# Optimization experiments

Measured on AMD Instinct MI355X. Metric: run time of the kernel, lower is better.

Reference implementation:

```python
import jax, jax.numpy as jnp
import numpy as np
import math

B, C, H, W, M = 8, 256, 128, 128, 7
EPS = 1e-08


def setup_inputs() -> dict:
    key = jax.random.key(0)
    ks = jax.random.split(key, 7)
    x_high = jax.random.normal(ks[0], (B, C, H // 2, W // 2), jnp.float32)
    x_low = jax.random.normal(ks[1], (B, C, H, W), jnp.float32)
    w1 = jax.random.normal(ks[2], (32, M * M), jnp.float32) / np.sqrt(M * M)
    b1 = jnp.zeros((32,), jnp.float32)
    w2 = jax.random.normal(ks[3], (3, 32), jnp.float32) / np.sqrt(32)
    b2 = jnp.zeros((3,), jnp.float32)
    refine_w = jax.random.normal(ks[4], (C, C), jnp.float32) / np.sqrt(C)
    return {"x_high": x_high, "x_low": x_low, "w1": w1, "b1": b1,
            "w2": w2, "b2": b2, "refine_w": refine_w}


def _anisotropic_kernel(params):
    # params: (B,3) -> normalized Gaussian kernels (B, m, m)
    theta = jnp.arctan2(params[:, 0], params[:, 1]) / 2.0 + math.pi / 2.0
    lam1 = jnp.exp(params[:, 2])
    lam2 = 1.0 / (lam1 + EPS)
    coords = jnp.arange(M, dtype=jnp.float32) - (M // 2)  # -3..3
    yy = coords[:, None]  # (m,1) varies along rows (torch meshgrid 'ij')
    xx = coords[None, :]  # (1,m)
    cos_t = jnp.cos(theta)[:, None, None]
    sin_t = jnp.sin(theta)[:, None, None]
    x_rot = xx * cos_t + yy * sin_t          # (B,m,m)
    y_rot = -xx * sin_t + yy * cos_t
    l1 = lam1[:, None, None]
    l2 = lam2[:, None, None]
    k = jnp.exp(-(x_rot ** 2 / (2.0 * l1 ** 2) + y_rot ** 2 / (2.0 * l2 ** 2)))
    return k / (jnp.sum(k, axis=(1, 2), keepdims=True) + EPS)


def _depthwise(x, kern):
    # x: (B,C,H,W), kern: (B,m,m) -> per-sample depthwise conv, kernel shared across C
    k = jnp.repeat(kern, C, axis=0)[:, None, :, :]  # (B*C,1,m,m)
    pad = M // 2
    y = jax.lax.conv_general_dilated(
        x.reshape(1, B * C, H, W), k, (1, 1), [(pad, pad), (pad, pad)],
        dimension_numbers=("NCHW", "OIHW", "NCHW"), feature_group_count=B * C)
    return y.reshape(B, C, H, W)


def reference(x_high, x_low, w1, b1, w2, b2, refine_w):
    # bilinear upsample (align_corners=False == half-pixel, matches jax.image.resize)
    x_high_up = jax.image.resize(x_high, (B, C, H, W), method="bilinear")

    x_f = jnp.fft.fftshift(jnp.fft.fft2(x_low, norm="ortho"), axes=(-2, -1))
    real, imag = jnp.real(x_f), jnp.imag(x_f)
    mag = jnp.abs(x_f)
    mag_weighted = jnp.mean(mag, axis=1, keepdims=True)  # (B,1,H,W)
    h0, w0 = H // 2 - M // 2, W // 2 - M // 2
    mag_center = mag_weighted[:, :, h0:h0 + M, w0:w0 + M]  # (B,1,m,m)

    # param_net: Flatten -> Linear -> ReLU -> Linear
    flat = mag_center.reshape(B, M * M)
    h = jax.nn.relu(flat @ w1.T + b1)
    params = h @ w2.T + b2  # (B,3)

    kern = _anisotropic_kernel(params)
    real_f = _depthwise(real, kern)
    imag_f = _depthwise(imag, kern)

    # 1x1 refine conv (bias-free), shared for real and imag parts
    real_f = jnp.einsum("bchw,oc->bohw", real_f, refine_w)
    imag_f = jnp.einsum("bchw,oc->bohw", imag_f, refine_w)

    out_f = jax.lax.complex(real_f, imag_f)
    out_f = jnp.fft.ifftshift(out_f, axes=(-2, -1))
    x_low_enhanced = jnp.real(jnp.fft.ifft2(out_f, norm="ortho"))
    return x_low_enhanced + x_high_up
```

## Files before the change

### kernel.cpp

```cpp
#include <hip/hip_runtime.h>

typedef __attribute__((ext_vector_type(8))) short bf16x8;
typedef __attribute__((ext_vector_type(4))) float f32x4;
typedef __attribute__((ext_vector_type(4))) int   i32x4;

#define PI_F 3.14159265358979323846f
#define C128 0.0490873852123405f
#define INV_SQRT128 0.0883883476483184f
#define INV128 0.0078125f

#define NB 8
#define NC 256
#define NH 128
#define NW 128
#define IMG 16384
#define NIMG 2048

#define GH_STRIDE 3200
#define AB_STRIDE 3072

__device__ __forceinline__ unsigned short f2bf(float f){
  unsigned int u = __float_as_uint(f);
  u += 0x7FFFu + ((u >> 16) & 1u);
  return (unsigned short)(u >> 16);
}
__device__ __forceinline__ float bf2f(unsigned short u){
  return __uint_as_float(((unsigned int)u) << 16);
}

__device__ __constant__ int c_pcnt[6] = {1,2,3,3,2,1};
__device__ __constant__ int c_pdp0[6] = {6,5,4,0,0,0};

__global__ void __launch_bounds__(256) K1(const float* __restrict__ xlow,
                                          float* __restrict__ GH){
  __shared__ unsigned short xs[128*132];
  __shared__ float Hlo[4][2][128];
  __shared__ float Hhi[4][2][128];
  __shared__ float Gg [4][2][128];
  __shared__ float twc[128], tws[128];

  const int tid = threadIdx.x;
  const int img = blockIdx.x;
  float* ghb = GH + (size_t)img*GH_STRIDE;

  if (tid < 128){
    float s,c; __sincosf((float)tid*C128, &s, &c);
    twc[tid]=c; tws[tid]=s;
  }
  {
    const float4* xp = (const float4*)(xlow + (size_t)img*IMG);
    #pragma unroll
    for (int k=0; k<16; ++k){
      int e4 = k*256 + tid;
      float4 v = xp[e4];
      int px = e4*4;
      int r = px >> 7, c = px & 127;
      ushort4 u; u.x=f2bf(v.x); u.y=f2bf(v.y); u.z=f2bf(v.z); u.w=f2bf(v.w);
      *(ushort4*)(&xs[r*132 + c]) = u;
    }
  }
  __syncthreads();

  const float w1c= 0.9987954562051724f, w1s=-0.0490676743274180f;
  const float w2c= 0.9951847266721969f, w2s=-0.0980171403295606f;
  const float w3c= 0.9891765099647810f, w3s=-0.1467304744553617f;
  const float v1c=-0.9891765099647810f, v1s=-0.1467304744553617f;
  const float v2c=-0.9951847266721969f, v2s=-0.0980171403295606f;
  const float v3c=-0.9987954562051724f, v3s=-0.0490676743274180f;

  if (tid < 128){
    const int r = tid;
    const unsigned short* xr = &xs[r*132];
    float h0=0.f, h64=0.f;
    float aR1=0,aI1=0,aR2=0,aI2=0,aR3=0,aI3=0;
    float bR1=0,bI1=0,bR2=0,bI2=0,bR3=0,bI3=0;
    float t1c=1,t1s=0,t2c=1,t2s=0,t3c=1,t3s=0;
    float u1c=1,u1s=0,u2c=1,u2s=0,u3c=1,u3s=0;
    for (int c=0;c<128;++c){
      float xv = bf2f(xr[c]);
      h0 += xv;
      h64 += (c&1)? -xv : xv;
      aR1 += xv*t1c; aI1 += xv*t1s;
      aR2 += xv*t2c; aI2 += xv*t2s;
      aR3 += xv*t3c; aI3 += xv*t3s;
      bR1 += xv*u1c; bI1 += xv*u1s;
      bR2 += xv*u2c; bI2 += xv*u2s;
      bR3 += xv*u3c; bI3 += xv*u3s;
      float t;
      t = t1c*w1c - t1s*w1s; t1s = t1c*w1s + t1s*w1c; t1c = t;
      t = t2c*w2c - t2s*w2s; t2s = t2c*w2s + t2s*w2c; t2c = t;
      t = t3c*w3c - t3s*w3s; t3s = t3c*w3s + t3s*w3c; t3c = t;
      t = u1c*v1c - u1s*v1s; u1s = u1c*v1s + u1s*v1c; u1c = t;
      t = u2c*v2c - u2s*v2s; u2s = u2c*v2s + u2s*v2c; u2c = t;
      t = u3c*v3c - u3s*v3s; u3s = u3c*v3s + u3s*v3c; u3c = t;
    }
    Hlo[0][0][r]=h0;  Hlo[0][1][r]=0.f;
    Hlo[1][0][r]=aR1; Hlo[1][1][r]=aI1;
    Hlo[2][0][r]=aR2; Hlo[2][1][r]=aI2;
    Hlo[3][0][r]=aR3; Hlo[3][1][r]=aI3;
    Hhi[0][0][r]=bR1; Hhi[0][1][r]=bI1;
    Hhi[1][0][r]=bR2; Hhi[1][1][r]=bI2;
    Hhi[2][0][r]=bR3; Hhi[2][1][r]=bI3;
    Hhi[3][0][r]=h64; Hhi[3][1][r]=0.f;
  } else {
    const int c = tid - 128;
    float g64=0.f;
    float bR1=0,bI1=0,bR2=0,bI2=0,bR3=0,bI3=0;
    float u1c=1,u1s=0,u2c=1,u2s=0,u3c=1,u3s=0;
    for (int r=0;r<128;++r){
      float xv = bf2f(xs[r*132 + c]);
      g64 += (r&1)? -xv : xv;
      bR1 += xv*u1c; bI1 += xv*u1s;
      bR2 += xv*u2c; bI2 += xv*u2s;
      bR3 += xv*u3c; bI3 += xv*u3s;
      float t;
      t = u1c*v1c - u1s*v1s; u1s = u1c*v1s + u1s*v1c; u1c = t;
      t = u2c*v2c - u2s*v2s; u2s = u2c*v2s + u2s*v2c; u2c = t;
      t = u3c*v3c - u3s*v3s; u3s = u3c*v3s + u3s*v3c; u3c = t;
    }
    Gg[0][0][c]=bR1; Gg[0][1][c]=bI1;
    Gg[1][0][c]=bR2; Gg[1][1][c]=bI2;
    Gg[2][0][c]=bR3; Gg[2][1][c]=bI3;
    Gg[3][0][c]=g64; Gg[3][1][c]=0.f;
  }
  __syncthreads();

  #pragma unroll
  for (int k=0;k<6;++k){
    int idx = k*256 + tid;
    int w = idx >> 8, reim = (idx >> 7) & 1, c = idx & 127;
    float sg = reim ? -1.f : 1.f;
    float vG, vH;
    if (w < 4){ vG = Gg[w][reim][c];  vH = Hhi[w][reim][c]; }
    else if (w == 4){ vG = sg*Gg[2][reim][c]; vH = sg*Hhi[2][reim][c]; }
    else { vG = sg*Gg[1][reim][c]; vH = sg*Hhi[1][reim][c]; }
    ghb[idx]        = vG * INV_SQRT128;
    ghb[1536 + idx] = vH * INV_SQRT128;
  }
  if (tid < 36){
    int wi = tid/6, zi = tid%6;
    int z = 61 + zi;
    float fR=0.f, fI=0.f;
    for (int c=0;c<128;++c){
      float gR, gI;
      if (wi < 4){ gR = Gg[wi][0][c]; gI = Gg[wi][1][c]; }
      else if (wi == 4){ gR = Gg[2][0][c]; gI = -Gg[2][1][c]; }
      else { gR = Gg[1][0][c]; gI = -Gg[1][1][c]; }
      int m = (z*c) & 127;
      float tc = twc[m], ts = tws[m];
      fR += gR*tc + gI*ts;
      fI += gI*tc - gR*ts;
    }
    ghb[3072 + tid*2]     = fR * INV128;
    ghb[3072 + tid*2 + 1] = fI * INV128;
  }
  if (tid >= 64 && tid < 113){
    int i = tid - 64;
    int u = i/7 - 3, v = i%7 - 3;
    int va = v < 0 ? -v : v;
    float vsg = v < 0 ? -1.f : 1.f;
    float fR=0.f, fI=0.f;
    for (int r=0;r<128;++r){
      float hR = Hlo[va][0][r], hI = vsg*Hlo[va][1][r];
      int m = ((u*r) % 128 + 128) & 127;
      float tc = twc[m], ts = tws[m];
      fR += hR*tc + hI*ts;
      fI += hI*tc - hR*ts;
    }
    fR *= INV128; fI *= INV128;
    ghb[3144 + i] = sqrtf(fR*fR + fI*fI);
  }
}

__global__ void __launch_bounds__(64) K_mlp(const float* __restrict__ GH,
                                            const float* __restrict__ w1,
                                            const float* __restrict__ b1,
                                            const float* __restrict__ w2,
                                            const float* __restrict__ b2,
                                            float* __restrict__ kern){
  __shared__ float flat[49];
  __shared__ float hh[32];
  const int b = blockIdx.x, tid = threadIdx.x;
  if (tid < 49){
    float s = 0.f;
    for (int c=0; c<256; ++c)
      s += GH[(size_t)(b*256 + c)*GH_STRIDE + 3144 + tid];
    flat[tid] = s * (1.0f/256.0f);
  }
  __syncthreads();
  if (tid < 32){
    float s = b1[tid];
    for (int i=0; i<49; ++i) s += flat[i]*w1[tid*49+i];
    hh[tid] = fmaxf(s, 0.f);
  }
  __syncthreads();
  if (tid == 0){
    float p[3];
    #pragma unroll
    for (int k=0; k<3; ++k){
      float s = b2[k];
      for (int j=0; j<32; ++j) s += hh[j]*w2[k*32+j];
      p[k] = s;
    }
    float theta = atan2f(p[0], p[1])*0.5f + 1.57079632679489662f;
    float ct = cosf(theta), st = sinf(theta);
    float l1 = expf(p[2]);
    float l2 = 1.0f/(l1 + 1e-8f);
    float inv1 = 1.0f/(2.0f*l1*l1);
    float inv2 = 1.0f/(2.0f*l2*l2);
    float sum = 0.f;
    for (int i=0; i<7; ++i) for (int j=0; j<7; ++j){
      float yy = (float)(i-3), xx = (float)(j-3);
      float xr =  xx*ct + yy*st;
      float yr = -xx*st + yy*ct;
      sum += expf(-(xr*xr*inv1 + yr*yr*inv2));
    }
    float inv = 1.0f/(sum + 1e-8f);
    for (int i=0; i<7; ++i) for (int j=0; j<7; ++j){
      float yy = (float)(i-3), xx = (float)(j-3);
      float xr =  xx*ct + yy*st;
      float yr = -xx*st + yy*ct;
      kern[b*49 + i*7 + j] = expf(-(xr*xr*inv1 + yr*yr*inv2)) * inv;
    }
  }
}

__global__ void __launch_bounds__(256) K3(const float* __restrict__ kern,
                                          float* __restrict__ KL,
                                          float* __restrict__ W){
  __shared__ float twc[128], tws[128], kl[49];
  __shared__ float kapl[7][2][128];
  const int b = blockIdx.x, tid = threadIdx.x;
  if (tid < 128){
    float s,c; __sincosf((float)tid*C128, &s, &c);
    twc[tid]=c; tws[tid]=s;
  }
  if (tid < 49) kl[tid] = kern[b*49 + tid];
  __syncthreads();
  if (tid < 128){
    const int c = tid;
    float* klb = KL + (size_t)b*3584;
    #pragma unroll
    for (int dp=0; dp<7; ++dp){
      float kR=0.f, kI=0.f;
      #pragma unroll
      for (int dq=0; dq<7; ++dq){
        int m = (((dq-3)*c) % 128 + 128) & 127;
        float kv = kl[dp*7+dq];
        kR += kv*twc[m]; kI -= kv*tws[m];
      }
      klb[(dp*2  )*128 + c] = kR;
      klb[(dp*2+1)*128 + c] = kI;
      kapl[dp][0][c] = kR; kapl[dp][1][c] = kI;
    }
    const int r = tid;
    #pragma unroll
    for (int dq=0; dq<7; ++dq){
      float lR=0.f, lI=0.f;
      #pragma unroll
      for (int dp=0; dp<7; ++dp){
        int m = (((dp-3)*r) % 128 + 128) & 127;
        float kv = kl[dp*7+dq];
        lR += kv*twc[m]; lI -= kv*tws[m];
      }
      klb[1792 + (dq*2  )*128 + r] = lR;
      klb[1792 + (dq*2+1)*128 + r] = lI;
    }
  }
  __syncthreads();
  for (int k=0;k<64;++k){
    int px = k*256 + tid;
    int r = px >> 7, c = px & 127;
    float w = 0.f;
    #pragma unroll
    for (int dp=0; dp<7; ++dp){
      int m = (((dp-3)*r) % 128 + 128) & 127;
      w += twc[m]*kapl[dp][0][c] + tws[m]*kapl[dp][1][c];
    }
    W[(size_t)b*IMG + px] = w;
  }
}

__global__ void __launch_bounds__(128) K_tab(const float* __restrict__ GH,
                                             const float* __restrict__ KL,
                                             const float* __restrict__ kern,
                                             float* __restrict__ AB){
  __shared__ float dRe[36], dIm[36], kl[49];
  const int tid = threadIdx.x;
  const int img = blockIdx.x, b = img >> 8;
  const float* ghb = GH + (size_t)img*GH_STRIDE;
  const float* klb = KL + (size_t)b*3584;
  float* abb = AB + (size_t)img*AB_STRIDE;

  if (tid < 49) kl[tid] = kern[b*49 + tid];
  __syncthreads();
  if (tid < 36){
    int si = tid/6, ti = tid%6;
    float dR=0.f, dI=0.f;
    for (int j=0; j<c_pcnt[si]; ++j){
      int dp = c_pdp0[si] + j;
      int wi = (si-3) + dp;
      for (int l=0; l<c_pcnt[ti]; ++l){
        int dq = c_pdp0[ti] + l;
        int zi = (ti-3) + dq;
        float kv = kl[dp*7+dq];
        dR += kv * ghb[3072 + (wi*6+zi)*2];
        dI += kv * ghb[3072 + (wi*6+zi)*2 + 1];
      }
    }
    dRe[tid] = dR; dIm[tid] = dI;
  }
  __syncthreads();

  const int c = tid;
  float s1,c1; __sincosf((float)c*C128, &s1, &c1);
  float c2 = c1*c1 - s1*s1, s2 = 2.f*c1*s1;
  float c3 = c1*c2 - s1*s2, s3 = s1*c2 + c1*s2;
  float ct[6] = {c3,c2,c1,1.f,c1,c2};
  float st[6] = {-s3,-s2,-s1,0.f,s1,s2};
  float sgnc = (c & 1) ? -1.f : 1.f;

  float gr[6], gi[6], kr[7], ki[7];
  #pragma unroll
  for (int w=0;w<6;++w){ gr[w]=ghb[(w*2)*128+c]; gi[w]=ghb[(w*2+1)*128+c]; }
  #pragma unroll
  for (int dp=0;dp<7;++dp){ kr[dp]=klb[(dp*2)*128+c]; ki[dp]=klb[(dp*2+1)*128+c]; }

  #pragma unroll
  for (int si=0; si<6; ++si){
    float dR=0.f, dI=0.f;
    for (int j=0; j<c_pcnt[si]; ++j){
      int dp = c_pdp0[si] + j;
      int w = (si-3) + dp;
      dR += kr[dp]*gr[w] - ki[dp]*gi[w];
      dI += kr[dp]*gi[w] + ki[dp]*gr[w];
    }
    float corrR=0.f, corrI=0.f;
    #pragma unroll
    for (int ti=0; ti<6; ++ti){
      float DR = dRe[si*6+ti], DI = dIm[si*6+ti];
      corrR += DR*ct[ti] - DI*st[ti];
      corrI += DR*st[ti] + DI*ct[ti];
    }
    abb[(si*2  )*128 + c] = INV_SQRT128*dR - INV128*sgnc*corrR;
    abb[(si*2+1)*128 + c] = INV_SQRT128*dI - INV128*sgnc*corrI;
  }

  const int r = tid;
  float hr[6], hi_[6], lr[7], li[7];
  #pragma unroll
  for (int z=0;z<6;++z){ hr[z]=ghb[1536+(z*2)*128+r]; hi_[z]=ghb[1536+(z*2+1)*128+r]; }
  #pragma unroll
  for (int dq=0;dq<7;++dq){ lr[dq]=klb[1792+(dq*2)*128+r]; li[dq]=klb[1792+(dq*2+1)*128+r]; }
  #pragma unroll
  for (int ti=0; ti<6; ++ti){
    float bR=0.f, bI=0.f;
    for (int l=0; l<c_pcnt[ti]; ++l){
      int dq = c_pdp0[ti] + l;
      int z = (ti-3) + dq;
      bR += lr[dq]*hr[z] - li[dq]*hi_[z];
      bI += lr[dq]*hi_[z] + li[dq]*hr[z];
    }
    abb[1536 + r*12 + ti*2]     = INV_SQRT128*bR;
    abb[1536 + r*12 + ti*2 + 1] = INV_SQRT128*bI;
  }
}

__global__ void __launch_bounds__(256) K4(const float* __restrict__ xlow,
                                          const float* __restrict__ W,
                                          const float* __restrict__ AB,
                                          unsigned short* __restrict__ filt){
  const int tid = threadIdx.x;
  const int img = blockIdx.x, b = img >> 8;
  const int c0 = (tid & 63)*2, grp = tid >> 6;
  const float* abb = AB + (size_t)img*AB_STRIDE;
  const float* xim = xlow + (size_t)img*IMG;
  const float* Wb  = W + (size_t)b*IMG;
  unsigned short* fim = filt + (size_t)img*IMG;

  float ar[2][6], ai[2][6], ctc[2][6], stc[2][6];
  #pragma unroll
  for (int col=0; col<2; ++col){
    int c = c0 + col;
    #pragma unroll
    for (int si=0;si<6;++si){ ar[col][si]=abb[(si*2)*128+c]; ai[col][si]=abb[(si*2+1)*128+c]; }
    float s1,c1; __sincosf((float)c*C128, &s1, &c1);
    float c2 = c1*c1 - s1*s1, s2 = 2.f*c1*s1;
    float c3 = c1*c2 - s1*s2, s3 = s1*c2 + c1*s2;
    ctc[col][0]=c3; ctc[col][1]=c2; ctc[col][2]=c1; ctc[col][3]=1.f; ctc[col][4]=c1; ctc[col][5]=c2;
    stc[col][0]=-s3; stc[col][1]=-s2; stc[col][2]=-s1; stc[col][3]=0.f; stc[col][4]=s1; stc[col][5]=s2;
  }

  for (int k=0;k<32;++k){
    int ru = __builtin_amdgcn_readfirstlane(grp*32 + k);
    const float* brow = abb + 1536 + ru*12;
    float4 b0 = *(const float4*)(brow);
    float4 b1 = *(const float4*)(brow+4);
    float4 b2 = *(const float4*)(brow+8);
    float rs1,rc1; __sincosf((float)ru*C128, &rs1, &rc1);
    float rc2 = rc1*rc1 - rs1*rs1, rs2 = 2.f*rc1*rs1;
    float rc3 = rc1*rc2 - rs1*rs2, rs3 = rs1*rc2 + rc1*rs2;
    float rcs[6] = {rc3,rc2,rc1,1.f,rc1,rc2};
    float rss[6] = {-rs3,-rs2,-rs1,0.f,rs1,rs2};

    float ER0 = 0.f, ER1 = 0.f;
    #pragma unroll
    for (int si=0;si<6;++si){
      ER0 += rcs[si]*ar[0][si] - rss[si]*ai[0][si];
      ER1 += rcs[si]*ar[1][si] - rss[si]*ai[1][si];
    }
    float rsg = (ru & 1) ? -1.f : 1.f;
    ER0 *= rsg; ER1 *= rsg;

    float bRv[6] = {b0.x, b0.z, b1.x, b1.z, b2.x, b2.z};
    float bIv[6] = {b0.y, b0.w, b1.y, b1.w, b2.y, b2.w};
    float EC0 = 0.f, EC1 = 0.f;
    #pragma unroll
    for (int ti=0;ti<6;++ti){
      EC0 += ctc[0][ti]*bRv[ti] - stc[0][ti]*bIv[ti];
      EC1 += ctc[1][ti]*bRv[ti] - stc[1][ti]*bIv[ti];
    }
    int px = ru*128 + c0;
    float2 xv = *(const float2*)(&xim[px]);
    float2 wv = *(const float2*)(&Wb[px]);
    float v0 = xv.x*wv.x - ER0 - EC0;
    float v1 = xv.y*wv.y - ER1 + EC1;
    unsigned int pack = ((unsigned int)f2bf(v1) << 16) | (unsigned int)f2bf(v0);
    *(unsigned int*)(&fim[px]) = pack;
  }
}

__global__ void __launch_bounds__(256) K_w(const float* __restrict__ rw,
                                           unsigned short* __restrict__ rwbf){
  int i = blockIdx.x*256 + threadIdx.x;
  rwbf[i] = f2bf(rw[i]);
}

__global__ void __launch_bounds__(256) K_up(const float* __restrict__ xhigh,
                                            unsigned short* __restrict__ up){
  __shared__ float xs[64*68];
  const int tid = threadIdx.x;
  const int img = blockIdx.x;
  const float* src = xhigh + (size_t)img*4096;
  unsigned short* dst = up + (size_t)img*IMG;

  #pragma unroll
  for (int p=0; p<4; ++p){
    int t = p*256 + tid;
    float4 v = ((const float4*)src)[t];
    int r = t >> 4, k = t & 15;
    *(float4*)(&xs[r*68 + k*4]) = v;
  }
  __syncthreads();

  for (int k=0; k<32; ++k){
    int pr = k*256 + tid;
    int y = pr >> 6, x0 = (pr & 63)*2;
    float fy = 0.5f*(float)y - 0.25f;
    int iyf = (int)floorf(fy);
    float ty = fy - (float)iyf;
    int iy0 = iyf < 0 ? 0 : iyf;
    int iy1 = (iyf+1) > 63 ? 63 : (iyf+1);
    float wy1 = ty, wy0 = 1.0f - ty;
    const float* r0 = &xs[iy0*68];
    const float* r1 = &xs[iy1*68];

    float outv[2];
    #pragma unroll
    for (int e=0; e<2; ++e){
      int x = x0 + e;
      float fx = 0.5f*(float)x - 0.25f;
      int ixf = (int)floorf(fx);
      float tx = fx - (float)ixf;
      int ix0 = ixf < 0 ? 0 : ixf;
      int ix1 = (ixf+1) > 63 ? 63 : (ixf+1);
      float wx1 = tx, wx0 = 1.0f - tx;
      outv[e] = wy0*(wx0*r0[ix0] + wx1*r0[ix1])
              + wy1*(wx0*r1[ix0] + wx1*r1[ix1]);
    }
    unsigned int pack = ((unsigned int)f2bf(outv[1]) << 16) | (unsigned int)f2bf(outv[0]);
    *(unsigned int*)(&dst[y*NW + x0]) = pack;
  }
}

__global__ void __launch_bounds__(256) K_trans(const unsigned short* __restrict__ in,
                                               unsigned short* __restrict__ outT){
  __shared__ unsigned short tile[32][33];
  const int p0 = blockIdx.x * 32;
  const int c0 = blockIdx.y * 32;
  const int b  = blockIdx.z;
  const int tx = threadIdx.x & 31, ty = threadIdx.x >> 5;
  #pragma unroll
  for (int w=0; w<4; ++w){
    int ii = ty + w*8;
    tile[ii][tx] = in[((size_t)b*NC + c0 + ii)*IMG + p0 + tx];
  }
  __syncthreads();
  #pragma unroll
  for (int w=0; w<4; ++w){
    int ii = ty + w*8;
    outT[((size_t)b*IMG + p0 + ii)*NC + c0 + tx] = tile[tx][ii];
  }
}

__global__ void __launch_bounds__(256) K_gemm(const unsigned short* __restrict__ rwbf,
                                              const unsigned short* __restrict__ filtT,
                                              const unsigned short* __restrict__ up,
                                              float* __restrict__ out){
  __shared__ unsigned short At[128*32];
  __shared__ unsigned short Bt[128*32];
  const int tid = threadIdx.x, lane = tid & 63, wv = tid >> 6;
  const int wr = wv >> 1, wc = wv & 1;
  const int xg = blockIdx.x;
  const int g16 = xg >> 4, i16 = xg & 15;
  const int ot = i16 >> 3, pt = (g16 << 3) | (i16 & 7);
  const int b = blockIdx.z;
  const int p0 = pt*128, o0 = ot*128;

  f32x4 acc[4][4];
  #pragma unroll
  for (int m=0;m<4;++m)
    #pragma unroll
    for (int n=0;n<4;++n){ f32x4 z = {0.f,0.f,0.f,0.f}; acc[m][n] = z; }

  const int row  = tid >> 2;
  const int koff = (tid & 3) * 8;

  for (int ks=0; ks<8; ++ks){
    const int k0 = ks*32;
    i32x4 av0 = *(const i32x4*)(&rwbf[(size_t)(o0+row   )*256 + k0 + koff]);
    i32x4 av1 = *(const i32x4*)(&rwbf[(size_t)(o0+row+64)*256 + k0 + koff]);
    i32x4 bv0 = *(const i32x4*)(&filtT[((size_t)b*IMG + p0+row   )*256 + k0 + koff]);
    i32x4 bv1 = *(const i32x4*)(&filtT[((size_t)b*IMG + p0+row+64)*256 + k0 + koff]);
    __syncthreads();
    *(i32x4*)(&At[ row     *32 + koff]) = av0;
    *(i32x4*)(&At[(row+64) *32 + koff]) = av1;
    *(i32x4*)(&Bt[ row     *32 + koff]) = bv0;
    *(i32x4*)(&Bt[(row+64) *32 + koff]) = bv1;
    __syncthreads();

    const int g = lane >> 4, r16 = lane & 15;
    bf16x8 af[4], bfr[4];
    #pragma unroll
    for (int m=0;m<4;++m) af[m]  = *(const bf16x8*)(&At[(wr*64 + m*16 + r16)*32 + g*8]);
    #pragma unroll
    for (int n=0;n<4;++n) bfr[n] = *(const bf16x8*)(&Bt[(wc*64 + n*16 + r16)*32 + g*8]);
    #pragma unroll
    for (int m=0;m<4;++m)
      #pragma unroll
      for (int n=0;n<4;++n)
        acc[m][n] = __builtin_amdgcn_mfma_f32_16x16x32_bf16(af[m], bfr[n], acc[m][n], 0, 0, 0);
  }

  const int y = pt;
  const int g = lane >> 4, r16 = lane & 15;
  #pragma unroll
  for (int m=0;m<4;++m){
    #pragma unroll
    for (int j=0;j<4;++j){
      int o = o0 + wr*64 + m*16 + g*4 + j;
      size_t base = (size_t)(b*NC + o)*IMG + (size_t)y*NW;
      #pragma unroll
      for (int n=0;n<4;++n){
        int xcol = wc*64 + n*16 + r16;
        float upv = bf2f(up[base + xcol]);
        out[base + xcol] = acc[m][n][j] + upv;
      }
    }
  }
}

extern "C" void kernel_launch(void* const* d_in, const int* in_sizes, int n_in,
                              void* d_out, int out_size, void* d_ws, size_t ws_size,
                              hipStream_t stream){
  (void)in_sizes; (void)n_in; (void)out_size; (void)ws_size;
  const float* xhigh = (const float*)d_in[0];
  const float* xlow  = (const float*)d_in[1];
  const float* w1    = (const float*)d_in[2];
  const float* b1    = (const float*)d_in[3];
  const float* w2    = (const float*)d_in[4];
  const float* b2    = (const float*)d_in[5];
  const float* rw    = (const float*)d_in[6];

  char* ws = (char*)d_ws;
  unsigned short* filt  = (unsigned short*)(ws);
  unsigned short* filtT = (unsigned short*)(ws + 67108864);
  float* GH   = (float*)(ws + 134217728);
  float* AB   = (float*)(ws + 160432128);
  float* kern = (float*)(ws + 185597952);
  float* KL   = (float*)(ws + 185602048);
  float* Wf   = (float*)(ws + 185716736);
  unsigned short* rwbf = (unsigned short*)(ws + 186241024);
  unsigned short* up   = filt;

  K1   <<<NIMG, 256, 0, stream>>>(xlow, GH);
  K_mlp<<<NB,   64,  0, stream>>>(GH, w1, b1, w2, b2, kern);
  K3   <<<NB,   256, 0, stream>>>(kern, KL, Wf);
  K_w  <<<256,  256, 0, stream>>>(rw, rwbf);
  K_tab<<<NIMG, 128, 0, stream>>>(GH, KL, kern, AB);
  K4   <<<NIMG, 256, 0, stream>>>(xlow, Wf, AB, filt);
  K_trans<<<dim3(512, 8, NB), 256, 0, stream>>>(filt, filtT);
  K_up <<<NIMG, 256, 0, stream>>>(xhigh, up);
  K_gemm <<<dim3(256, 1, NB), 256, 0, stream>>>(rwbf, filtT, up, (float*)d_out);
}
```

Before: 356.4 us.

## Speed up row DFT recurrence, widen transpose tiles, double-buffer GEMM LDS

K1's partial DFT now splits each row or column into even and odd samples and uses a Chebyshev recurrence for the twiddles. This derives the high-frequency bins from the low-frequency sums by symmetry, which cuts the number of accumulators and twiddle rotations. K_trans moves to 64x64 tiles with vectorized ushort4 loads and stores. K_gemm double-buffers its LDS tiles, so global loads for the next k-step overlap the MFMAs and one barrier per iteration is removed. The changes trade extra register and LDS use for less ALU work, fewer memory transactions and fewer syncs, and the new twiddle recurrence may accumulate slightly more error.

```diff
diff --git a/kernel.cpp b/kernel.cpp
--- a/kernel.cpp
+++ b/kernel.cpp
@@ -15,6 +15,7 @@
 #define NW 128
 #define IMG 16384
 #define NIMG 2048
+#define XST 130
 
 #define GH_STRIDE 3200
 #define AB_STRIDE 3072
@@ -31,9 +32,13 @@
 __device__ __constant__ int c_pcnt[6] = {1,2,3,3,2,1};
 __device__ __constant__ int c_pdp0[6] = {6,5,4,0,0,0};
 
+#define COS1 0.9987954562051724f
+#define SIN1 0.0490676743274180f
+#define K1CH (2.0f*COS1)
+
 __global__ void __launch_bounds__(256) K1(const float* __restrict__ xlow,
                                           float* __restrict__ GH){
-  __shared__ unsigned short xs[128*132];
+  __shared__ unsigned short xs[128*XST];
   __shared__ float Hlo[4][2][128];
   __shared__ float Hhi[4][2][128];
   __shared__ float Gg [4][2][128];
@@ -55,73 +60,105 @@
       float4 v = xp[e4];
       int px = e4*4;
       int r = px >> 7, c = px & 127;
-      ushort4 u; u.x=f2bf(v.x); u.y=f2bf(v.y); u.z=f2bf(v.z); u.w=f2bf(v.w);
-      *(ushort4*)(&xs[r*132 + c]) = u;
-    }
-  }
-  __syncthreads();
-
-  const float w1c= 0.9987954562051724f, w1s=-0.0490676743274180f;
-  const float w2c= 0.9951847266721969f, w2s=-0.0980171403295606f;
-  const float w3c= 0.9891765099647810f, w3s=-0.1467304744553617f;
-  const float v1c=-0.9891765099647810f, v1s=-0.1467304744553617f;
-  const float v2c=-0.9951847266721969f, v2s=-0.0980171403295606f;
-  const float v3c=-0.9987954562051724f, v3s=-0.0490676743274180f;
+      unsigned int pw0 = (unsigned int)f2bf(v.x) | ((unsigned int)f2bf(v.y) << 16);
+      unsigned int pw1 = (unsigned int)f2bf(v.z) | ((unsigned int)f2bf(v.w) << 16);
+      *(unsigned int*)(&xs[r*XST + c    ]) = pw0;
+      *(unsigned int*)(&xs[r*XST + c + 2]) = pw1;
+    }
+  }
+  __syncthreads();
+
+  float A0e=0.f, A0o=0.f;
+  float Ce1=0.f,Se1=0.f,Co1=0.f,So1=0.f;
+  float Ce2=0.f,Se2=0.f,Co2=0.f,So2=0.f;
+  float Ce3=0.f,Se3=0.f,Co3=0.f,So3=0.f;
 
   if (tid < 128){
     const int r = tid;
-    const unsigned short* xr = &xs[r*132];
-    float h0=0.f, h64=0.f;
-    float aR1=0,aI1=0,aR2=0,aI2=0,aR3=0,aI3=0;
-    float bR1=0,bI1=0,bR2=0,bI2=0,bR3=0,bI3=0;
-    float t1c=1,t1s=0,t2c=1,t2s=0,t3c=1,t3s=0;
-    float u1c=1,u1s=0,u2c=1,u2s=0,u3c=1,u3s=0;
-    for (int c=0;c<128;++c){
-      float xv = bf2f(xr[c]);
-      h0 += xv;
-      h64 += (c&1)? -xv : xv;
-      aR1 += xv*t1c; aI1 += xv*t1s;
-      aR2 += xv*t2c; aI2 += xv*t2s;
-      aR3 += xv*t3c; aI3 += xv*t3s;
-      bR1 += xv*u1c; bI1 += xv*u1s;
-      bR2 += xv*u2c; bI2 += xv*u2s;
-      bR3 += xv*u3c; bI3 += xv*u3s;
-      float t;
-      t = t1c*w1c - t1s*w1s; t1s = t1c*w1s + t1s*w1c; t1c = t;
-      t = t2c*w2c - t2s*w2s; t2s = t2c*w2s + t2s*w2c; t2c = t;
-      t = t3c*w3c - t3s*w3s; t3s = t3c*w3s + t3s*w3c; t3c = t;
-      t = u1c*v1c - u1s*v1s; u1s = u1c*v1s + u1s*v1c; u1c = t;
-      t = u2c*v2c - u2s*v2s; u2s = u2c*v2s + u2s*v2c; u2c = t;
-      t = u3c*v3c - u3s*v3s; u3s = u3c*v3s + u3s*v3c; u3c = t;
-    }
-    Hlo[0][0][r]=h0;  Hlo[0][1][r]=0.f;
-    Hlo[1][0][r]=aR1; Hlo[1][1][r]=aI1;
-    Hlo[2][0][r]=aR2; Hlo[2][1][r]=aI2;
-    Hlo[3][0][r]=aR3; Hlo[3][1][r]=aI3;
-    Hhi[0][0][r]=bR1; Hhi[0][1][r]=bI1;
-    Hhi[1][0][r]=bR2; Hhi[1][1][r]=bI2;
-    Hhi[2][0][r]=bR3; Hhi[2][1][r]=bI3;
-    Hhi[3][0][r]=h64; Hhi[3][1][r]=0.f;
+    const unsigned short* xr = &xs[r*XST];
+    float cp = 1.f, sp = 0.f;
+    float cn = COS1, sn = SIN1;
+    #pragma unroll 4
+    for (int j=0; j<64; ++j){
+      unsigned int pk = *(const unsigned int*)(&xr[2*j]);
+      float xe = __uint_as_float(pk << 16);
+      float xo = __uint_as_float(pk & 0xffff0000u);
+      {
+        float t2 = cp + cp;
+        float c2 = fmaf(t2, cp, -1.f);
+        float s2 = t2 * sp;
+        float c3 = fmaf(t2, c2, -cp);
+        float s3 = fmaf(t2, s2, -sp);
+        A0e += xe;
+        Ce1 = fmaf(xe, cp, Ce1); Se1 = fmaf(xe, sp, Se1);
+        Ce2 = fmaf(xe, c2, Ce2); Se2 = fmaf(xe, s2, Se2);
+        Ce3 = fmaf(xe, c3, Ce3); Se3 = fmaf(xe, s3, Se3);
+      }
+      {
+        float t2 = cn + cn;
+        float c2 = fmaf(t2, cn, -1.f);
+        float s2 = t2 * sn;
+        float c3 = fmaf(t2, c2, -cn);
+        float s3 = fmaf(t2, s2, -sn);
+        A0o += xo;
+        Co1 = fmaf(xo, cn, Co1); So1 = fmaf(xo, sn, So1);
+        Co2 = fmaf(xo, c2, Co2); So2 = fmaf(xo, s2, So2);
+        Co3 = fmaf(xo, c3, Co3); So3 = fmaf(xo, s3, So3);
+      }
+      float cpn = fmaf(K1CH, cn, -cp);
+      float spn = fmaf(K1CH, sn, -sp);
+      float cnn = fmaf(K1CH, cpn, -cn);
+      float snn = fmaf(K1CH, spn, -sn);
+      cp = cpn; sp = spn; cn = cnn; sn = snn;
+    }
+    Hlo[0][0][r]=A0e+A0o;  Hlo[0][1][r]=0.f;
+    Hlo[1][0][r]=Ce1+Co1;  Hlo[1][1][r]=-(Se1+So1);
+    Hlo[2][0][r]=Ce2+Co2;  Hlo[2][1][r]=-(Se2+So2);
+    Hlo[3][0][r]=Ce3+Co3;  Hlo[3][1][r]=-(Se3+So3);
+    Hhi[0][0][r]=Ce3-Co3;  Hhi[0][1][r]=Se3-So3;
+    Hhi[1][0][r]=Ce2-Co2;  Hhi[1][1][r]=Se2-So2;
+    Hhi[2][0][r]=Ce1-Co1;  Hhi[2][1][r]=Se1-So1;
+    Hhi[3][0][r]=A0e-A0o;  Hhi[3][1][r]=0.f;
   } else {
     const int c = tid - 128;
-    float g64=0.f;
-    float bR1=0,bI1=0,bR2=0,bI2=0,bR3=0,bI3=0;
-    float u1c=1,u1s=0,u2c=1,u2s=0,u3c=1,u3s=0;
-    for (int r=0;r<128;++r){
-      float xv = bf2f(xs[r*132 + c]);
-      g64 += (r&1)? -xv : xv;
-      bR1 += xv*u1c; bI1 += xv*u1s;
-      bR2 += xv*u2c; bI2 += xv*u2s;
-      bR3 += xv*u3c; bI3 += xv*u3s;
-      float t;
-      t = u1c*v1c - u1s*v1s; u1s = u1c*v1s + u1s*v1c; u1c = t;
-      t = u2c*v2c - u2s*v2s; u2s = u2c*v2s + u2s*v2c; u2c = t;
-      t = u3c*v3c - u3s*v3s; u3s = u3c*v3s + u3s*v3c; u3c = t;
-    }
-    Gg[0][0][c]=bR1; Gg[0][1][c]=bI1;
-    Gg[1][0][c]=bR2; Gg[1][1][c]=bI2;
-    Gg[2][0][c]=bR3; Gg[2][1][c]=bI3;
-    Gg[3][0][c]=g64; Gg[3][1][c]=0.f;
+    float cp = 1.f, sp = 0.f;
+    float cn = COS1, sn = SIN1;
+    #pragma unroll 4
+    for (int j=0; j<64; ++j){
+      float xe = bf2f(xs[(2*j  )*XST + c]);
+      float xo = bf2f(xs[(2*j+1)*XST + c]);
+      {
+        float t2 = cp + cp;
+        float c2 = fmaf(t2, cp, -1.f);
+        float s2 = t2 * sp;
+        float c3 = fmaf(t2, c2, -cp);
+        float s3 = fmaf(t2, s2, -sp);
+        A0e += xe;
+        Ce1 = fmaf(xe, cp, Ce1); Se1 = fmaf(xe, sp, Se1);
+        Ce2 = fmaf(xe, c2, Ce2); Se2 = fmaf(xe, s2, Se2);
+        Ce3 = fmaf(xe, c3, Ce3); Se3 = fmaf(xe, s3, Se3);
+      }
+      {
+        float t2 = cn + cn;
+        float c2 = fmaf(t2, cn, -1.f);
+        float s2 = t2 * sn;
+        float c3 = fmaf(t2, c2, -cn);
+        float s3 = fmaf(t2, s2, -sn);
+        A0o += xo;
+        Co1 = fmaf(xo, cn, Co1); So1 = fmaf(xo, sn, So1);
+        Co2 = fmaf(xo, c2, Co2); So2 = fmaf(xo, s2, So2);
+        Co3 = fmaf(xo, c3, Co3); So3 = fmaf(xo, s3, So3);
+      }
+      float cpn = fmaf(K1CH, cn, -cp);
+      float spn = fmaf(K1CH, sn, -sp);
+      float cnn = fmaf(K1CH, cpn, -cn);
+      float snn = fmaf(K1CH, spn, -sn);
+      cp = cpn; sp = spn; cn = cnn; sn = snn;
+    }
+    Gg[0][0][c]=Ce3-Co3;  Gg[0][1][c]=Se3-So3;
+    Gg[1][0][c]=Ce2-Co2;  Gg[1][1][c]=Se2-So2;
+    Gg[2][0][c]=Ce1-Co1;  Gg[2][1][c]=Se1-So1;
+    Gg[3][0][c]=A0e-A0o;  Gg[3][1][c]=0.f;
   }
   __syncthreads();
 
@@ -485,21 +522,29 @@
 
 __global__ void __launch_bounds__(256) K_trans(const unsigned short* __restrict__ in,
                                                unsigned short* __restrict__ outT){
-  __shared__ unsigned short tile[32][33];
-  const int p0 = blockIdx.x * 32;
-  const int c0 = blockIdx.y * 32;
+  __shared__ unsigned short tile[64*68];
+  const int p0 = blockIdx.x * 64;
+  const int c0 = blockIdx.y * 64;
   const int b  = blockIdx.z;
-  const int tx = threadIdx.x & 31, ty = threadIdx.x >> 5;
-  #pragma unroll
-  for (int w=0; w<4; ++w){
-    int ii = ty + w*8;
-    tile[ii][tx] = in[((size_t)b*NC + c0 + ii)*IMG + p0 + tx];
-  }
-  __syncthreads();
-  #pragma unroll
-  for (int w=0; w<4; ++w){
-    int ii = ty + w*8;
-    outT[((size_t)b*IMG + p0 + ii)*NC + c0 + tx] = tile[tx][ii];
+  const int tid = threadIdx.x;
+  const int lo = tid >> 4;
+  const int q4 = (tid & 15) * 4;
+
+  #pragma unroll
+  for (int pass=0; pass<4; ++pass){
+    int cc = lo + pass*16;
+    ushort4 v = *(const ushort4*)(&in[((size_t)b*NC + c0 + cc)*IMG + p0 + q4]);
+    tile[(q4+0)*68 + cc] = v.x;
+    tile[(q4+1)*68 + cc] = v.y;
+    tile[(q4+2)*68 + cc] = v.z;
+    tile[(q4+3)*68 + cc] = v.w;
+  }
+  __syncthreads();
+  #pragma unroll
+  for (int pass=0; pass<4; ++pass){
+    int pp = lo + pass*16;
+    ushort4 v = *(const ushort4*)(&tile[pp*68 + q4]);
+    *(ushort4*)(&outT[((size_t)b*IMG + p0 + pp)*NC + c0 + q4]) = v;
   }
 }
 
@@ -507,8 +552,8 @@
                                               const unsigned short* __restrict__ filtT,
                                               const unsigned short* __restrict__ up,
                                               float* __restrict__ out){
-  __shared__ unsigned short At[128*32];
-  __shared__ unsigned short Bt[128*32];
+  __shared__ unsigned short At[2][128*32];
+  __shared__ unsigned short Bt[2][128*32];
   const int tid = threadIdx.x, lane = tid & 63, wv = tid >> 6;
   const int wr = wv >> 1, wc = wv & 1;
   const int xg = blockIdx.x;
@@ -525,35 +570,52 @@
 
   const int row  = tid >> 2;
   const int koff = (tid & 3) * 8;
-
+  const unsigned short* aP0 = &rwbf[(size_t)(o0+row   )*256 + koff];
+  const unsigned short* aP1 = &rwbf[(size_t)(o0+row+64)*256 + koff];
+  const unsigned short* bP0 = &filtT[((size_t)b*IMG + p0+row   )*256 + koff];
+  const unsigned short* bP1 = &filtT[((size_t)b*IMG + p0+row+64)*256 + koff];
+
+  i32x4 av0 = *(const i32x4*)(aP0);
+  i32x4 av1 = *(const i32x4*)(aP1);
+  i32x4 bv0 = *(const i32x4*)(bP0);
+  i32x4 bv1 = *(const i32x4*)(bP1);
+  *(i32x4*)(&At[0][ row     *32 + koff]) = av0;
+  *(i32x4*)(&At[0][(row+64) *32 + koff]) = av1;
+  *(i32x4*)(&Bt[0][ row     *32 + koff]) = bv0;
+  *(i32x4*)(&Bt[0][(row+64) *32 + koff]) = bv1;
+  __syncthreads();
+
+  const int g = lane >> 4, r16 = lane & 15;
   for (int ks=0; ks<8; ++ks){
-    const int k0 = ks*32;
-    i32x4 av0 = *(const i32x4*)(&rwbf[(size_t)(o0+row   )*256 + k0 + koff]);
-    i32x4 av1 = *(const i32x4*)(&rwbf[(size_t)(o0+row+64)*256 + k0 + koff]);
-    i32x4 bv0 = *(const i32x4*)(&filtT[((size_t)b*IMG + p0+row   )*256 + k0 + koff]);
-    i32x4 bv1 = *(const i32x4*)(&filtT[((size_t)b*IMG + p0+row+64)*256 + k0 + koff]);
-    __syncthreads();
-    *(i32x4*)(&At[ row     *32 + koff]) = av0;
-    *(i32x4*)(&At[(row+64) *32 + koff]) = av1;
-    *(i32x4*)(&Bt[ row     *32 + koff]) = bv0;
-    *(i32x4*)(&Bt[(row+64) *32 + koff]) = bv1;
-    __syncthreads();
-
-    const int g = lane >> 4, r16 = lane & 15;
+    const int cur = ks & 1;
+    if (ks < 7){
+      const int k0 = (ks+1)*32;
+      av0 = *(const i32x4*)(aP0 + k0);
+      av1 = *(const i32x4*)(aP1 + k0);
+      bv0 = *(const i32x4*)(bP0 + k0);
+      bv1 = *(const i32x4*)(bP1 + k0);
+    }
     bf16x8 af[4], bfr[4];
     #pragma unroll
-    for (int m=0;m<4;++m) af[m]  = *(const bf16x8*)(&At[(wr*64 + m*16 + r16)*32 + g*8]);
-    #pragma unroll
-    for (int n=0;n<4;++n) bfr[n] = *(const bf16x8*)(&Bt[(wc*64 + n*16 + r16)*32 + g*8]);
+    for (int m=0;m<4;++m) af[m]  = *(const bf16x8*)(&At[cur][(wr*64 + m*16 + r16)*32 + g*8]);
+    #pragma unroll
+    for (int n=0;n<4;++n) bfr[n] = *(const bf16x8*)(&Bt[cur][(wc*64 + n*16 + r16)*32 + g*8]);
     #pragma unroll
     for (int m=0;m<4;++m)
       #pragma unroll
       for (int n=0;n<4;++n)
         acc[m][n] = __builtin_amdgcn_mfma_f32_16x16x32_bf16(af[m], bfr[n], acc[m][n], 0, 0, 0);
+    if (ks < 7){
+      const int nxt = cur ^ 1;
+      *(i32x4*)(&At[nxt][ row     *32 + koff]) = av0;
+      *(i32x4*)(&At[nxt][(row+64) *32 + koff]) = av1;
+      *(i32x4*)(&Bt[nxt][ row     *32 + koff]) = bv0;
+      *(i32x4*)(&Bt[nxt][(row+64) *32 + koff]) = bv1;
+      __syncthreads();
+    }
   }
 
   const int y = pt;
-  const int g = lane >> 4, r16 = lane & 15;
   #pragma unroll
   for (int m=0;m<4;++m){
     #pragma unroll
@@ -599,7 +661,7 @@
   K_w  <<<256,  256, 0, stream>>>(rw, rwbf);
   K_tab<<<NIMG, 128, 0, stream>>>(GH, KL, kern, AB);
   K4   <<<NIMG, 256, 0, stream>>>(xlow, Wf, AB, filt);
-  K_trans<<<dim3(512, 8, NB), 256, 0, stream>>>(filt, filtT);
+  K_trans<<<dim3(256, 4, NB), 256, 0, stream>>>(filt, filtT);
   K_up <<<NIMG, 256, 0, stream>>>(xhigh, up);
   K_gemm <<<dim3(256, 1, NB), 256, 0, stream>>>(rwbf, filtT, up, (float*)d_out);
 }
```

Result: faster. 314.1 us (-11.9%).
